# Optimization experiments

Measured on AMD Instinct MI355X. Metric: run time of the kernel, lower is better.

## Reference

```python
import jax, jax.numpy as jnp
import numpy as np

N_NODES = 50000
N_EDGES = 800000
IN_C, HID_C, OUT_C = 512, 256, 128


def setup_inputs() -> dict:
    key = jax.random.key(0)
    k1, k2, k3, k4, k5, k6 = jax.random.split(key, 6)
    x = jax.random.normal(k1, (N_NODES, IN_C), dtype=jnp.float32)
    edge_index = jax.random.randint(k2, (2, N_EDGES), 0, N_NODES, dtype=jnp.int64)
    # Glorot-ish init for linear weights, zero bias (PyG GCNConv default)
    W1 = jax.random.normal(k3, (IN_C, HID_C), dtype=jnp.float32) / np.sqrt(IN_C)
    b1 = jnp.zeros((HID_C,), dtype=jnp.float32)
    W2 = jax.random.normal(k4, (HID_C, OUT_C), dtype=jnp.float32) / np.sqrt(HID_C)
    b2 = jnp.zeros((OUT_C,), dtype=jnp.float32)
    return {"x": x, "edge_index": edge_index, "W1": W1, "b1": b1, "W2": W2, "b2": b2}


def _gcn_layer(h, src, dst, norm, W, b, n_nodes):
    # h: [N, Fin] -> [N, Fout];  out_i = sum_{j->i} norm_e * (h W)_j + b
    h = h @ W
    msg = h[src] * norm[:, None]            # [E+N, Fout]
    out = jax.ops.segment_sum(msg, dst, num_segments=n_nodes)
    return out + b


def reference(x, edge_index, W1, b1, W2, b2):
    n = x.shape[0]
    loops = jnp.arange(n, dtype=edge_index.dtype)
    src = jnp.concatenate([edge_index[0], loops])  # add self-loops
    dst = jnp.concatenate([edge_index[1], loops])
    # symmetric normalization D^{-1/2} (A+I) D^{-1/2}
    deg = jax.ops.segment_sum(jnp.ones_like(src, dtype=x.dtype), dst, num_segments=n)
    dinv = jax.lax.rsqrt(jnp.maximum(deg, 1.0))
    norm = dinv[src] * dinv[dst]

    h = _gcn_layer(x, src, dst, norm, W1, b1, n)
    h = jax.nn.relu(h)
    # dropout: identity in eval mode (training=False)
    out = _gcn_layer(h, src, dst, norm, W2, b2, n)
    return out
```

## Files before the change

### kernel.cpp

```cpp
#include <hip/hip_runtime.h>
#include <hip/hip_bf16.h>

#define N_NODES 50000
#define N_EDGES 800000
#define IN_C 512
#define HID_C 256
#define OUT_C 128
#define SCAN_BLOCKS 49

typedef short bf16x8 __attribute__((ext_vector_type(8)));
typedef float f32x4 __attribute__((ext_vector_type(4)));

__device__ __forceinline__ float bf2f(unsigned short u) {
    return __uint_as_float(((unsigned)u) << 16);
}
__device__ __forceinline__ unsigned short f2bf(float f) {
    __hip_bfloat16 h = __float2bfloat16(f);
    return *(unsigned short*)&h;
}

__global__ void zero_counts_kernel(int* __restrict__ counts) {
    int i = blockIdx.x * blockDim.x + threadIdx.x;
    if (i < N_NODES) counts[i] = 0;
}

__global__ void count_kernel(const int* __restrict__ ei, int* __restrict__ counts) {
    int e = blockIdx.x * blockDim.x + threadIdx.x;
    if (e < N_EDGES) atomicAdd(&counts[ei[N_EDGES + e]], 1);
}

__global__ __launch_bounds__(256) void scan_part_kernel(const int* __restrict__ counts,
                                                        int* __restrict__ excl,
                                                        int* __restrict__ bsums) {
    __shared__ int tsum[256];
    const int t = threadIdx.x;
    const int base = blockIdx.x * 1024 + t * 4;
    int v[4];
    int s = 0;
#pragma unroll
    for (int j = 0; j < 4; j++) {
        int idx = base + j;
        v[j] = (idx < N_NODES) ? counts[idx] : 0;
        s += v[j];
    }
    tsum[t] = s;
    __syncthreads();
    for (int off = 1; off < 256; off <<= 1) {
        int add = (t >= off) ? tsum[t - off] : 0;
        __syncthreads();
        tsum[t] += add;
        __syncthreads();
    }
    int run = tsum[t] - s;
#pragma unroll
    for (int j = 0; j < 4; j++) {
        int idx = base + j;
        if (idx < N_NODES) excl[idx] = run;
        run += v[j];
    }
    if (t == 255) bsums[blockIdx.x] = tsum[255];
}

__global__ void scan_sums_kernel(int* __restrict__ bsums) {
    int ln = threadIdx.x;
    int v = (ln < SCAN_BLOCKS) ? bsums[ln] : 0;
    for (int off = 1; off < 64; off <<= 1) {
        int u = __shfl_up(v, off, 64);
        if (ln >= off) v += u;
    }
    int excl = __shfl_up(v, 1, 64);
    if (ln == 0) excl = 0;
    if (ln < SCAN_BLOCKS) bsums[ln] = excl;
}

__global__ void add_dinv_kernel(int* __restrict__ offsets, const int* __restrict__ bsums,
                                int* __restrict__ woff, const int* __restrict__ counts,
                                float* __restrict__ dinv) {
    int i = blockIdx.x * blockDim.x + threadIdx.x;
    if (i < N_NODES) {
        int o = offsets[i] + bsums[i >> 10];
        offsets[i] = o;
        woff[i] = o;
        dinv[i] = rsqrtf(1.0f + (float)counts[i]);
    }
    if (i == 0) offsets[N_NODES] = N_EDGES;
}

__global__ void fill_kernel(const int* __restrict__ ei, int* __restrict__ woff,
                            const float* __restrict__ dinv,
                            int* __restrict__ sorted_src, float* __restrict__ sorted_w) {
    int e = blockIdx.x * blockDim.x + threadIdx.x;
    if (e < N_EDGES) {
        int s = ei[e];
        int d = ei[N_EDGES + e];
        int pos = atomicAdd(&woff[d], 1);
        sorted_src[pos] = s;
        sorted_w[pos] = dinv[s];
    }
}

__global__ __launch_bounds__(256) void cast_x_kernel(const float* __restrict__ x,
                                                     unsigned short* __restrict__ xb) {
    size_t i = ((size_t)blockIdx.x * 256 + threadIdx.x) * 4;
    float4 v = *(const float4*)&x[i];
    ushort4 o;
    o.x = f2bf(v.x); o.y = f2bf(v.y); o.z = f2bf(v.z); o.w = f2bf(v.w);
    *(ushort4*)&xb[i] = o;
}

__global__ __launch_bounds__(256) void tcast_kernel(const float* __restrict__ W,
                                                    unsigned short* __restrict__ WT,
                                                    int K, int N) {
    int idx = blockIdx.x * 256 + threadIdx.x;
    int n = idx / K, k = idx - n * K;
    WT[idx] = f2bf(W[(size_t)k * N + n]);
}

__global__ __launch_bounds__(256) void mfma_gemm_bt(const unsigned short* __restrict__ A,
                                                    const unsigned short* __restrict__ BT,
                                                    unsigned short* __restrict__ C,
                                                    int M, int N, int K) {
    __shared__ unsigned short As[128 * 32];
    __shared__ unsigned short Bs[128 * 32];

    const int tid = threadIdx.x;
    const int w = tid >> 6;
    const int ln = tid & 63;
    const int br = blockIdx.y * 128;
    const int bc = blockIdx.x * 128;

    const int quad = ln >> 4;
    const int l16 = ln & 15;
    const int wr = (w >> 1) * 64;
    const int wc = (w & 1) * 64;

    const int crow = ln >> 2;
    const int koff = (ln & 3) * 8;

    f32x4 acc[4][4];
#pragma unroll
    for (int mt = 0; mt < 4; mt++)
#pragma unroll
        for (int nt = 0; nt < 4; nt++) acc[mt][nt] = (f32x4){0.f, 0.f, 0.f, 0.f};

    for (int kk = 0; kk < K; kk += 32) {
#pragma unroll
        for (int t = 0; t < 2; t++) {
            int c = w + t * 4;
            int row = br + c * 16 + crow;
            row = row < M ? row : M - 1;
            const unsigned short* gp = A + (size_t)row * K + kk + koff;
            unsigned short* lp = As + c * 512 + ln * 8;
            __builtin_amdgcn_global_load_lds((const __attribute__((address_space(1))) void*)gp,
                                             (__attribute__((address_space(3))) void*)lp,
                                             16, 0, 0);
        }
#pragma unroll
        for (int t = 0; t < 2; t++) {
            int c = w + t * 4;
            int row = bc + c * 16 + crow;
            const unsigned short* gp = BT + (size_t)row * K + kk + koff;
            unsigned short* lp = Bs + c * 512 + ln * 8;
            __builtin_amdgcn_global_load_lds((const __attribute__((address_space(1))) void*)gp,
                                             (__attribute__((address_space(3))) void*)lp,
                                             16, 0, 0);
        }
        __syncthreads();

        bf16x8 af[4], bfr[4];
#pragma unroll
        for (int mt = 0; mt < 4; mt++)
            af[mt] = *(const bf16x8*)&As[(wr + mt * 16 + l16) * 32 + quad * 8];
#pragma unroll
        for (int nt = 0; nt < 4; nt++)
            bfr[nt] = *(const bf16x8*)&Bs[(wc + nt * 16 + l16) * 32 + quad * 8];
#pragma unroll
        for (int mt = 0; mt < 4; mt++)
#pragma unroll
            for (int nt = 0; nt < 4; nt++)
                acc[mt][nt] = __builtin_amdgcn_mfma_f32_16x16x32_bf16(af[mt], bfr[nt],
                                                                      acc[mt][nt], 0, 0, 0);
        __syncthreads();
    }

#pragma unroll
    for (int mt = 0; mt < 4; mt++) {
#pragma unroll
        for (int r = 0; r < 4; r++) {
            int gr = br + wr + mt * 16 + quad * 4 + r;
            if (gr < M) {
#pragma unroll
                for (int nt = 0; nt < 4; nt++) {
                    int gc = bc + wc + nt * 16 + l16;
                    C[(size_t)gr * N + gc] = f2bf(acc[mt][nt][r]);
                }
            }
        }
    }
}

template <int C, bool RELU, bool BF16_OUT>
__global__ __launch_bounds__(256) void gather_agg_kernel(const int* __restrict__ offsets,
                                                         const int* __restrict__ ssrc,
                                                         const float* __restrict__ sw,
                                                         const unsigned short* __restrict__ H,
                                                         const float* __restrict__ dinv,
                                                         const float* __restrict__ bias,
                                                         void* __restrict__ outv) {
    constexpr int G = C / 8;
    constexpr int NG = 64 / G;
    const int node = blockIdx.x * 4 + (threadIdx.x >> 6);
    if (node >= N_NODES) return;
    const int ln = threadIdx.x & 63;
    const int g = ln / G;
    const int l = ln % G;
    const int c0 = l * 8;
    const float di = dinv[node];

    float acc[8] = {};
    if (g == 0) {
        bf16x8 h = *(const bf16x8*)&H[(size_t)node * C + c0];
#pragma unroll
        for (int j = 0; j < 8; j++)
            acc[j] = di * di * bf2f((unsigned short)h[j]) + bias[c0 + j];
    }

    int k = offsets[node] + g;
    const int k1 = offsets[node + 1];
    for (; k + NG < k1; k += 2 * NG) {
        int s0 = ssrc[k], s1 = ssrc[k + NG];
        float w0 = di * sw[k], w1 = di * sw[k + NG];
        bf16x8 h0 = *(const bf16x8*)&H[(size_t)s0 * C + c0];
        bf16x8 h1 = *(const bf16x8*)&H[(size_t)s1 * C + c0];
#pragma unroll
        for (int j = 0; j < 8; j++)
            acc[j] += w0 * bf2f((unsigned short)h0[j]) + w1 * bf2f((unsigned short)h1[j]);
    }
    if (k < k1) {
        int s0 = ssrc[k];
        float w0 = di * sw[k];
        bf16x8 h0 = *(const bf16x8*)&H[(size_t)s0 * C + c0];
#pragma unroll
        for (int j = 0; j < 8; j++) acc[j] += w0 * bf2f((unsigned short)h0[j]);
    }

#pragma unroll
    for (int m = G; m < 64; m <<= 1) {
#pragma unroll
        for (int j = 0; j < 8; j++) acc[j] += __shfl_xor(acc[j], m, 64);
    }

    if (g == 0) {
        if (RELU) {
#pragma unroll
            for (int j = 0; j < 8; j++) acc[j] = fmaxf(acc[j], 0.0f);
        }
        if (BF16_OUT) {
            bf16x8 o;
#pragma unroll
            for (int j = 0; j < 8; j++) o[j] = (short)f2bf(acc[j]);
            *(bf16x8*)&((unsigned short*)outv)[(size_t)node * C + c0] = o;
        } else {
            float* out = (float*)outv;
            *(float4*)&out[(size_t)node * C + c0] = make_float4(acc[0], acc[1], acc[2], acc[3]);
            *(float4*)&out[(size_t)node * C + c0 + 4] = make_float4(acc[4], acc[5], acc[6], acc[7]);
        }
    }
}

extern "C" void kernel_launch(void* const* d_in, const int* in_sizes, int n_in,
                              void* d_out, int out_size, void* d_ws, size_t ws_size,
                              hipStream_t stream) {
    const float* x  = (const float*)d_in[0];
    const int*   ei = (const int*)d_in[1];
    const float* W1 = (const float*)d_in[2];
    const float* b1 = (const float*)d_in[3];
    const float* W2 = (const float*)d_in[4];
    const float* b2 = (const float*)d_in[5];
    float* out = (float*)d_out;

    int*   counts     = (int*)d_ws;
    int*   offsets    = counts + 50048;
    int*   woff       = offsets + 50052;
    int*   bsums      = woff + 50048;
    float* dinv       = (float*)(bsums + 64);
    int*   sorted_src = (int*)(dinv + 50048);
    float* sorted_w   = (float*)(sorted_src + 800000);
    unsigned short* W1T = (unsigned short*)(sorted_w + 800000);
    unsigned short* W2T = W1T + 131072;
    unsigned short* xb  = W2T + 32768;
    unsigned short* H1  = xb + (size_t)N_NODES * IN_C;
    unsigned short* A1b = xb;
    unsigned short* H2  = xb + (size_t)N_NODES * HID_C;

    zero_counts_kernel<<<(N_NODES + 255) / 256, 256, 0, stream>>>(counts);
    count_kernel<<<(N_EDGES + 255) / 256, 256, 0, stream>>>(ei, counts);
    scan_part_kernel<<<SCAN_BLOCKS, 256, 0, stream>>>(counts, offsets, bsums);
    scan_sums_kernel<<<1, 64, 0, stream>>>(bsums);
    add_dinv_kernel<<<(N_NODES + 255) / 256, 256, 0, stream>>>(offsets, bsums, woff, counts, dinv);
    fill_kernel<<<(N_EDGES + 255) / 256, 256, 0, stream>>>(ei, woff, dinv, sorted_src, sorted_w);

    cast_x_kernel<<<(N_NODES * IN_C) / 1024, 256, 0, stream>>>(x, xb);
    tcast_kernel<<<(IN_C * HID_C) / 256, 256, 0, stream>>>(W1, W1T, IN_C, HID_C);
    tcast_kernel<<<(HID_C * OUT_C) / 256, 256, 0, stream>>>(W2, W2T, HID_C, OUT_C);

    {
        dim3 grid(HID_C / 128, (N_NODES + 127) / 128);
        mfma_gemm_bt<<<grid, 256, 0, stream>>>(xb, W1T, H1, N_NODES, HID_C, IN_C);
    }
    gather_agg_kernel<HID_C, true, true><<<(N_NODES + 3) / 4, 256, 0, stream>>>(
        offsets, sorted_src, sorted_w, H1, dinv, b1, (void*)A1b);

    {
        dim3 grid(OUT_C / 128, (N_NODES + 127) / 128);
        mfma_gemm_bt<<<grid, 256, 0, stream>>>(A1b, W2T, H2, N_NODES, OUT_C, HID_C);
    }
    gather_agg_kernel<OUT_C, false, false><<<(N_NODES + 3) / 4, 256, 0, stream>>>(
        offsets, sorted_src, sorted_w, H2, dinv, b2, (void*)out);
}
```

Baseline: 431.5 us.

## Fold source-side normalization into GEMM epilogue and gather layer-1 features in FP8

The GEMM epilogue now pre-scales each output row by dinv[row], and the gather applies dinv[dst] once at the end. This removes the per-edge weight array and its loads, and shrinks the CSR fill. Layer-1 hidden features are stored as FP8 (e4m3) instead of bf16, halving gather bytes. The gather loops are also unrolled to four outstanding loads. FP8 storage of the hidden features adds precision loss that may push the result against the tolerance.

```diff
diff --git a/kernel.cpp b/kernel.cpp
--- a/kernel.cpp
+++ b/kernel.cpp
@@ -10,6 +10,7 @@
 
 typedef short bf16x8 __attribute__((ext_vector_type(8)));
 typedef float f32x4 __attribute__((ext_vector_type(4)));
+typedef float f32x2 __attribute__((ext_vector_type(2)));
 
 __device__ __forceinline__ float bf2f(unsigned short u) {
     return __uint_as_float(((unsigned)u) << 16);
@@ -17,6 +18,14 @@
 __device__ __forceinline__ unsigned short f2bf(float f) {
     __hip_bfloat16 h = __float2bfloat16(f);
     return *(unsigned short*)&h;
+}
+__device__ __forceinline__ void acc_fp8x4(int dw, float* a) {
+    f32x2 lo = __builtin_amdgcn_cvt_pk_f32_fp8(dw, false);
+    f32x2 hi = __builtin_amdgcn_cvt_pk_f32_fp8(dw, true);
+    a[0] += lo[0]; a[1] += lo[1]; a[2] += hi[0]; a[3] += hi[1];
+}
+__device__ __forceinline__ unsigned char f2fp8(float f) {
+    return (unsigned char)(__builtin_amdgcn_cvt_pk_fp8_f32(f, 0.0f, 0, false) & 0xff);
 }
 
 __global__ void zero_counts_kernel(int* __restrict__ counts) {
@@ -87,15 +96,13 @@
 }
 
 __global__ void fill_kernel(const int* __restrict__ ei, int* __restrict__ woff,
-                            const float* __restrict__ dinv,
-                            int* __restrict__ sorted_src, float* __restrict__ sorted_w) {
+                            int* __restrict__ sedge) {
     int e = blockIdx.x * blockDim.x + threadIdx.x;
     if (e < N_EDGES) {
         int s = ei[e];
         int d = ei[N_EDGES + e];
         int pos = atomicAdd(&woff[d], 1);
-        sorted_src[pos] = s;
-        sorted_w[pos] = dinv[s];
+        sedge[pos] = s;
     }
 }
 
@@ -116,9 +123,11 @@
     WT[idx] = f2bf(W[(size_t)k * N + n]);
 }
 
+template <bool FP8_OUT>
 __global__ __launch_bounds__(256) void mfma_gemm_bt(const unsigned short* __restrict__ A,
                                                     const unsigned short* __restrict__ BT,
-                                                    unsigned short* __restrict__ C,
+                                                    void* __restrict__ Cv,
+                                                    const float* __restrict__ dinv,
                                                     int M, int N, int K) {
     __shared__ unsigned short As[128 * 32];
     __shared__ unsigned short Bs[128 * 32];
@@ -189,82 +198,130 @@
         for (int r = 0; r < 4; r++) {
             int gr = br + wr + mt * 16 + quad * 4 + r;
             if (gr < M) {
+                float ds = dinv[gr];
 #pragma unroll
                 for (int nt = 0; nt < 4; nt++) {
                     int gc = bc + wc + nt * 16 + l16;
-                    C[(size_t)gr * N + gc] = f2bf(acc[mt][nt][r]);
+                    float v = ds * acc[mt][nt][r];
+                    if (FP8_OUT)
+                        ((unsigned char*)Cv)[(size_t)gr * N + gc] = f2fp8(v);
+                    else
+                        ((unsigned short*)Cv)[(size_t)gr * N + gc] = f2bf(v);
                 }
             }
         }
     }
 }
 
-template <int C, bool RELU, bool BF16_OUT>
-__global__ __launch_bounds__(256) void gather_agg_kernel(const int* __restrict__ offsets,
-                                                         const int* __restrict__ ssrc,
-                                                         const float* __restrict__ sw,
-                                                         const unsigned short* __restrict__ H,
-                                                         const float* __restrict__ dinv,
-                                                         const float* __restrict__ bias,
-                                                         void* __restrict__ outv) {
-    constexpr int G = C / 8;
-    constexpr int NG = 64 / G;
+__global__ __launch_bounds__(256) void gather1_fp8(const int* __restrict__ offsets,
+                                                   const int* __restrict__ sedge,
+                                                   const unsigned char* __restrict__ H,
+                                                   const float* __restrict__ dinv,
+                                                   const float* __restrict__ bias,
+                                                   unsigned short* __restrict__ out) {
     const int node = blockIdx.x * 4 + (threadIdx.x >> 6);
     if (node >= N_NODES) return;
     const int ln = threadIdx.x & 63;
-    const int g = ln / G;
-    const int l = ln % G;
+    const int g = ln >> 5;
+    const int l = ln & 31;
     const int c0 = l * 8;
-    const float di = dinv[node];
 
     float acc[8] = {};
     if (g == 0) {
-        bf16x8 h = *(const bf16x8*)&H[(size_t)node * C + c0];
-#pragma unroll
-        for (int j = 0; j < 8; j++)
-            acc[j] = di * di * bf2f((unsigned short)h[j]) + bias[c0 + j];
+        uint2 d = *(const uint2*)&H[(size_t)node * HID_C + c0];
+        acc_fp8x4((int)d.x, acc);
+        acc_fp8x4((int)d.y, acc + 4);
     }
 
     int k = offsets[node] + g;
     const int k1 = offsets[node + 1];
-    for (; k + NG < k1; k += 2 * NG) {
-        int s0 = ssrc[k], s1 = ssrc[k + NG];
-        float w0 = di * sw[k], w1 = di * sw[k + NG];
-        bf16x8 h0 = *(const bf16x8*)&H[(size_t)s0 * C + c0];
-        bf16x8 h1 = *(const bf16x8*)&H[(size_t)s1 * C + c0];
+    for (; k + 6 < k1; k += 8) {
+        int s0 = sedge[k], s1 = sedge[k + 2], s2 = sedge[k + 4], s3 = sedge[k + 6];
+        uint2 d0 = *(const uint2*)&H[(size_t)s0 * HID_C + c0];
+        uint2 d1 = *(const uint2*)&H[(size_t)s1 * HID_C + c0];
+        uint2 d2 = *(const uint2*)&H[(size_t)s2 * HID_C + c0];
+        uint2 d3 = *(const uint2*)&H[(size_t)s3 * HID_C + c0];
+        acc_fp8x4((int)d0.x, acc); acc_fp8x4((int)d0.y, acc + 4);
+        acc_fp8x4((int)d1.x, acc); acc_fp8x4((int)d1.y, acc + 4);
+        acc_fp8x4((int)d2.x, acc); acc_fp8x4((int)d2.y, acc + 4);
+        acc_fp8x4((int)d3.x, acc); acc_fp8x4((int)d3.y, acc + 4);
+    }
+    for (; k < k1; k += 2) {
+        int s0 = sedge[k];
+        uint2 d0 = *(const uint2*)&H[(size_t)s0 * HID_C + c0];
+        acc_fp8x4((int)d0.x, acc);
+        acc_fp8x4((int)d0.y, acc + 4);
+    }
+
+#pragma unroll
+    for (int j = 0; j < 8; j++) acc[j] += __shfl_xor(acc[j], 32, 64);
+
+    if (g == 0) {
+        const float di = dinv[node];
+        bf16x8 o;
 #pragma unroll
         for (int j = 0; j < 8; j++)
-            acc[j] += w0 * bf2f((unsigned short)h0[j]) + w1 * bf2f((unsigned short)h1[j]);
-    }
-    if (k < k1) {
-        int s0 = ssrc[k];
-        float w0 = di * sw[k];
-        bf16x8 h0 = *(const bf16x8*)&H[(size_t)s0 * C + c0];
-#pragma unroll
-        for (int j = 0; j < 8; j++) acc[j] += w0 * bf2f((unsigned short)h0[j]);
-    }
-
-#pragma unroll
-    for (int m = G; m < 64; m <<= 1) {
+            o[j] = (short)f2bf(fmaxf(di * acc[j] + bias[c0 + j], 0.0f));
+        *(bf16x8*)&out[(size_t)node * HID_C + c0] = o;
+    }
+}
+
+__global__ __launch_bounds__(256) void gather2_bf16(const int* __restrict__ offsets,
+                                                    const int* __restrict__ sedge,
+                                                    const unsigned short* __restrict__ H,
+                                                    const float* __restrict__ dinv,
+                                                    const float* __restrict__ bias,
+                                                    float* __restrict__ out) {
+    const int node = blockIdx.x * 4 + (threadIdx.x >> 6);
+    if (node >= N_NODES) return;
+    const int ln = threadIdx.x & 63;
+    const int g = ln >> 4;
+    const int l = ln & 15;
+    const int c0 = l * 8;
+
+    float acc[8] = {};
+    if (g == 0) {
+        bf16x8 h = *(const bf16x8*)&H[(size_t)node * OUT_C + c0];
+#pragma unroll
+        for (int j = 0; j < 8; j++) acc[j] = bf2f((unsigned short)h[j]);
+    }
+
+    int k = offsets[node] + g;
+    const int k1 = offsets[node + 1];
+    for (; k + 12 < k1; k += 16) {
+        int s0 = sedge[k], s1 = sedge[k + 4], s2 = sedge[k + 8], s3 = sedge[k + 12];
+        bf16x8 h0 = *(const bf16x8*)&H[(size_t)s0 * OUT_C + c0];
+        bf16x8 h1 = *(const bf16x8*)&H[(size_t)s1 * OUT_C + c0];
+        bf16x8 h2 = *(const bf16x8*)&H[(size_t)s2 * OUT_C + c0];
+        bf16x8 h3 = *(const bf16x8*)&H[(size_t)s3 * OUT_C + c0];
+#pragma unroll
+        for (int j = 0; j < 8; j++) {
+            acc[j] += bf2f((unsigned short)h0[j]);
+            acc[j] += bf2f((unsigned short)h1[j]);
+            acc[j] += bf2f((unsigned short)h2[j]);
+            acc[j] += bf2f((unsigned short)h3[j]);
+        }
+    }
+    for (; k < k1; k += 4) {
+        int s0 = sedge[k];
+        bf16x8 h0 = *(const bf16x8*)&H[(size_t)s0 * OUT_C + c0];
+#pragma unroll
+        for (int j = 0; j < 8; j++) acc[j] += bf2f((unsigned short)h0[j]);
+    }
+
+#pragma unroll
+    for (int m = 16; m < 64; m <<= 1) {
 #pragma unroll
         for (int j = 0; j < 8; j++) acc[j] += __shfl_xor(acc[j], m, 64);
     }
 
     if (g == 0) {
-        if (RELU) {
-#pragma unroll
-            for (int j = 0; j < 8; j++) acc[j] = fmaxf(acc[j], 0.0f);
-        }
-        if (BF16_OUT) {
-            bf16x8 o;
-#pragma unroll
-            for (int j = 0; j < 8; j++) o[j] = (short)f2bf(acc[j]);
-            *(bf16x8*)&((unsigned short*)outv)[(size_t)node * C + c0] = o;
-        } else {
-            float* out = (float*)outv;
-            *(float4*)&out[(size_t)node * C + c0] = make_float4(acc[0], acc[1], acc[2], acc[3]);
-            *(float4*)&out[(size_t)node * C + c0 + 4] = make_float4(acc[4], acc[5], acc[6], acc[7]);
-        }
+        const float di = dinv[node];
+        float o[8];
+#pragma unroll
+        for (int j = 0; j < 8; j++) o[j] = di * acc[j] + bias[c0 + j];
+        *(float4*)&out[(size_t)node * OUT_C + c0] = make_float4(o[0], o[1], o[2], o[3]);
+        *(float4*)&out[(size_t)node * OUT_C + c0 + 4] = make_float4(o[4], o[5], o[6], o[7]);
     }
 }
 
@@ -284,12 +341,11 @@
     int*   woff       = offsets + 50052;
     int*   bsums      = woff + 50048;
     float* dinv       = (float*)(bsums + 64);
-    int*   sorted_src = (int*)(dinv + 50048);
-    float* sorted_w   = (float*)(sorted_src + 800000);
-    unsigned short* W1T = (unsigned short*)(sorted_w + 800000);
+    int*   sedge      = (int*)(dinv + 50048);
+    unsigned short* W1T = (unsigned short*)(sedge + 800000);
     unsigned short* W2T = W1T + 131072;
     unsigned short* xb  = W2T + 32768;
-    unsigned short* H1  = xb + (size_t)N_NODES * IN_C;
+    unsigned char*  H1  = (unsigned char*)(xb + (size_t)N_NODES * IN_C);
     unsigned short* A1b = xb;
     unsigned short* H2  = xb + (size_t)N_NODES * HID_C;
 
@@ -298,7 +354,7 @@
     scan_part_kernel<<<SCAN_BLOCKS, 256, 0, stream>>>(counts, offsets, bsums);
     scan_sums_kernel<<<1, 64, 0, stream>>>(bsums);
     add_dinv_kernel<<<(N_NODES + 255) / 256, 256, 0, stream>>>(offsets, bsums, woff, counts, dinv);
-    fill_kernel<<<(N_EDGES + 255) / 256, 256, 0, stream>>>(ei, woff, dinv, sorted_src, sorted_w);
+    fill_kernel<<<(N_EDGES + 255) / 256, 256, 0, stream>>>(ei, woff, sedge);
 
     cast_x_kernel<<<(N_NODES * IN_C) / 1024, 256, 0, stream>>>(x, xb);
     tcast_kernel<<<(IN_C * HID_C) / 256, 256, 0, stream>>>(W1, W1T, IN_C, HID_C);
@@ -306,15 +362,15 @@
 
     {
         dim3 grid(HID_C / 128, (N_NODES + 127) / 128);
-        mfma_gemm_bt<<<grid, 256, 0, stream>>>(xb, W1T, H1, N_NODES, HID_C, IN_C);
-    }
-    gather_agg_kernel<HID_C, true, true><<<(N_NODES + 3) / 4, 256, 0, stream>>>(
-        offsets, sorted_src, sorted_w, H1, dinv, b1, (void*)A1b);
+        mfma_gemm_bt<true><<<grid, 256, 0, stream>>>(xb, W1T, (void*)H1, dinv,
+                                                     N_NODES, HID_C, IN_C);
+    }
+    gather1_fp8<<<(N_NODES + 3) / 4, 256, 0, stream>>>(offsets, sedge, H1, dinv, b1, A1b);
 
     {
         dim3 grid(OUT_C / 128, (N_NODES + 127) / 128);
-        mfma_gemm_bt<<<grid, 256, 0, stream>>>(A1b, W2T, H2, N_NODES, OUT_C, HID_C);
-    }
-    gather_agg_kernel<OUT_C, false, false><<<(N_NODES + 3) / 4, 256, 0, stream>>>(
-        offsets, sorted_src, sorted_w, H2, dinv, b2, (void*)out);
-}
+        mfma_gemm_bt<false><<<grid, 256, 0, stream>>>(A1b, W2T, (void*)H2, dinv,
+                                                      N_NODES, OUT_C, HID_C);
+    }
+    gather2_bf16<<<(N_NODES + 3) / 4, 256, 0, stream>>>(offsets, sedge, H2, dinv, b2, out);
+}
```

Result: faster. 403.3 us (-6.5%).
